# Optimization experiments

Hardware: AMD Instinct MI355X
Metric: run time of the kernel (lower is better)

The kernel has to match this reference:

```python
import jax, jax.numpy as jnp
import numpy as np

# Problem-size constants (match input_specs / init_kwargs)
B, D, H, W = 2, 128, 128, 128   # batch and spatial grid
N = 200_000                      # number of active (non-empty) voxels
CI, CO, K = 64, 64, 3            # channels and cubic kernel size
DIL = 1                          # dilation


def setup_inputs() -> dict:
    key = jax.random.key(0)
    k1, k2, k3 = jax.random.split(key, 3)
    # Unique active voxel coordinates (submanifold conv assumes unique sites).
    rng = np.random.default_rng(0)
    lin = rng.choice(B * D * H * W, size=N, replace=False)
    b, rem = np.divmod(lin, D * H * W)
    z, rem = np.divmod(rem, H * W)
    y, x = np.divmod(rem, W)
    coords = jnp.asarray(np.stack([b, z, y, x], axis=1).astype(np.int32))  # [N,4]
    feats = jax.random.normal(k1, (N, CI), dtype=jnp.float32)
    # kaiming-uniform-ish init, layout [Co, Kd, Kh, Kw, Ci] as in the module
    fan_in = CI * K * K * K
    bound = 1.0 / np.sqrt(fan_in)
    weight = jax.random.uniform(k2, (CO, K, K, K, CI), dtype=jnp.float32,
                                minval=-bound, maxval=bound)
    bias = jax.random.uniform(k3, (CO,), dtype=jnp.float32,
                              minval=-bound, maxval=bound)
    return {"feats": feats, "weight": weight, "bias": bias, "coords": coords}


def _build_grid(coords):
    """Dense voxel hash: linear cell id -> row index in feats (-1 if empty)."""
    n = coords.shape[0]
    lin = ((coords[:, 0] * D + coords[:, 1]) * H + coords[:, 2]) * W + coords[:, 3]
    grid = jnp.full((B * D * H * W,), -1, dtype=jnp.int32)
    return grid.at[lin].set(jnp.arange(n, dtype=jnp.int32))


def reference(feats, weight, bias, coords):
    # Submanifold sparse 3D conv: out[p] = bias + sum_k W[k] @ feats[p + dil*(k - center)]
    # (only where the neighbor voxel is active; output sites == input sites).
    n = feats.shape[0]
    grid = _build_grid(coords)
    c = K // 2
    bz, z0, y0, x0 = coords[:, 0], coords[:, 1], coords[:, 2], coords[:, 3]
    out = jnp.broadcast_to(bias.astype(feats.dtype), (n, CO))
    for kd in range(K):
        for kh in range(K):
            for kw in range(K):
                dz, dy, dx = DIL * (kd - c), DIL * (kh - c), DIL * (kw - c)
                nz, ny, nx = z0 + dz, y0 + dy, x0 + dx
                inb = (nz >= 0) & (nz < D) & (ny >= 0) & (ny < H) & (nx >= 0) & (nx < W)
                nlin = ((bz * D + jnp.clip(nz, 0, D - 1)) * H
                        + jnp.clip(ny, 0, H - 1)) * W + jnp.clip(nx, 0, W - 1)
                nidx = jnp.where(inb, grid[nlin], -1)          # rulebook for this offset
                valid = (nidx >= 0)[:, None]
                g = jnp.where(valid, feats[jnp.clip(nidx, 0)], 0.0)  # gather [N,Ci]
                out = out + jnp.einsum('nc,oc->no', g, weight[:, kd, kh, kw, :])
    return out
```

## Files before the change

### kernel.cpp

```cpp
#include <hip/hip_runtime.h>
#include <hip/hip_bf16.h>

#define BDIM 2
#define DDIM 128
#define HDIM 128
#define WDIM 128
#define CI 64
#define CO 64
#define NTAPS 27
#define GRID_CELLS (BDIM * DDIM * HDIM * WDIM)
#define NCBLK (GRID_CELLS / 256)

typedef __attribute__((ext_vector_type(8))) short short8;
typedef __attribute__((ext_vector_type(4))) float floatx4;

#define WT_OFF   ((size_t)16 << 20)
#define BCNT_OFF (WT_OFF + ((size_t)256 << 10))
#define ORD_OFF  (BCNT_OFF + ((size_t)64 << 10))

__device__ __forceinline__ unsigned short f2bf(float f) {
    unsigned int u = __float_as_uint(f);
    return (unsigned short)((u + 0x7FFFu + ((u >> 16) & 1u)) >> 16);
}

__global__ __launch_bounds__(256) void scatter_kernel(
    const int* __restrict__ coords, int* __restrict__ grid, int n) {
    int i = blockIdx.x * blockDim.x + threadIdx.x;
    if (i >= n) return;
    int4 c = ((const int4*)coords)[i];
    grid[((c.x * DDIM + c.y) * HDIM + c.z) * WDIM + c.w] = i;
}

__global__ __launch_bounds__(256) void wfrag_kernel(
    const float* __restrict__ weight, short8* __restrict__ wt8) {
    int idx = blockIdx.x * blockDim.x + threadIdx.x;
    if (idx >= NTAPS * 2 * 4 * 64) return;
    int l = idx & 63, ot = (idx >> 6) & 3, s = (idx >> 8) & 1, t = idx >> 9;
    int o = ot * 16 + (l & 15);
    int k0 = s * 32 + ((l >> 4) << 3);
    const float* src = weight + ((size_t)o * NTAPS + t) * CI + k0;
    short8 v;
#pragma unroll
    for (int j = 0; j < 8; ++j) v[j] = (short)f2bf(src[j]);
    wt8[idx] = v;
}

__global__ __launch_bounds__(256) void count_kernel(
    const int* __restrict__ grid, int* __restrict__ bcnt) {
    int i = blockIdx.x * 256 + threadIdx.x;
    unsigned long long b = __ballot(grid[i] >= 0);
    __shared__ int wc[4];
    if ((threadIdx.x & 63) == 0) wc[threadIdx.x >> 6] = __popcll(b);
    __syncthreads();
    if (threadIdx.x == 0) bcnt[blockIdx.x] = wc[0] + wc[1] + wc[2] + wc[3];
}

__global__ __launch_bounds__(1024) void scan_kernel(int* __restrict__ bcnt) {
    __shared__ int part[1024];
    int tid = threadIdx.x;
    int v[16], s = 0;
#pragma unroll
    for (int k = 0; k < 16; ++k) { v[k] = bcnt[tid * 16 + k]; s += v[k]; }
    part[tid] = s;
    __syncthreads();
    for (int off = 1; off < 1024; off <<= 1) {
        int t = (tid >= off) ? part[tid - off] : 0;
        __syncthreads();
        part[tid] += t;
        __syncthreads();
    }
    int ex = tid ? part[tid - 1] : 0;
#pragma unroll
    for (int k = 0; k < 16; ++k) { int nv = ex; ex += v[k]; bcnt[tid * 16 + k] = nv; }
}

__global__ __launch_bounds__(256) void emit_kernel(
    const int* __restrict__ grid, const int* __restrict__ boff,
    int* __restrict__ order) {
    int i = blockIdx.x * 256 + threadIdx.x;
    int v = grid[i];
    int lane = threadIdx.x & 63, w = threadIdx.x >> 6;
    unsigned long long b = __ballot(v >= 0);
    __shared__ int wc[4];
    if (lane == 0) wc[w] = __popcll(b);
    __syncthreads();
    int woff = 0;
    for (int k = 0; k < w; ++k) woff += wc[k];
    if (v >= 0) {
        int rank = __popcll(b & ((1ull << lane) - 1ull));
        order[boff[blockIdx.x] + woff + rank] = v;
    }
}

__global__ __launch_bounds__(256) void conv_kernel(
    const float* __restrict__ feats, const short8* __restrict__ wt8,
    const float* __restrict__ bias, const int* __restrict__ coords,
    const int* __restrict__ grid, const int* __restrict__ order,
    float* __restrict__ out, int n) {
    __shared__ short8 bs[3][512];
    int tid = threadIdx.x;
    int w = tid >> 6, l = tid & 63, quad = l >> 4, m = l & 15;
    int jrow = blockIdx.x * 64 + w * 16 + m;
    int j = jrow < n ? jrow : n - 1;
    int p = order[j];
    int4 c = ((const int4*)coords)[p];

    int pr[7];
#pragma unroll
    for (int i = 0; i < 7; ++i) {
        int t = 4 * i + quad;
        int v = -1;
        if (t < NTAPS) {
            int dz = t / 9 - 1, rem = t % 9;
            int dy = rem / 3 - 1, dx = rem % 3 - 1;
            int nz = c.y + dz, ny = c.z + dy, nx = c.w + dx;
            if (nz >= 0 && nz < DDIM && ny >= 0 && ny < HDIM &&
                nx >= 0 && nx < WDIM)
                v = grid[((c.x * DDIM + nz) * HDIM + ny) * WDIM + nx];
        }
        pr[i] = v;
    }

    floatx4 acc0 = {0.f, 0.f, 0.f, 0.f}, acc1 = acc0, acc2 = acc0, acc3 = acc0;
    float4 xA[4], xB[4];
    int vA = -1, vB = -1;

#define STAGE(t)                                                     \
    {                                                                \
        const short8* src = wt8 + (size_t)(t) * 512 + tid * 2;       \
        short8 s0 = src[0], s1 = src[1];                             \
        bs[(t) % 3][tid * 2] = s0;                                   \
        bs[(t) % 3][tid * 2 + 1] = s1;                               \
    }

#define GATHER(t, g, vv)                                             \
    {                                                                \
        int vsrc = pr[(t) >> 2];                                     \
        vv = __shfl(vsrc, (((t) & 3) << 4) | m);                     \
        g[0] = g[1] = g[2] = g[3] = float4{0.f, 0.f, 0.f, 0.f};      \
        if (vv >= 0) {                                               \
            const float4* ar =                                       \
                (const float4*)(feats + (size_t)vv * CI + quad * 8); \
            g[0] = ar[0]; g[1] = ar[1]; g[2] = ar[8]; g[3] = ar[9];  \
        }                                                            \
    }

#define COMPUTE(t, g, vv)                                                          \
    if (__ballot(vv >= 0) != 0ull) {                                               \
        union { short8 s; __hip_bfloat162 h[4]; } f0, f1;                          \
        f0.h[0] = __float22bfloat162_rn({g[0].x, g[0].y});                         \
        f0.h[1] = __float22bfloat162_rn({g[0].z, g[0].w});                         \
        f0.h[2] = __float22bfloat162_rn({g[1].x, g[1].y});                         \
        f0.h[3] = __float22bfloat162_rn({g[1].z, g[1].w});                         \
        f1.h[0] = __float22bfloat162_rn({g[2].x, g[2].y});                         \
        f1.h[1] = __float22bfloat162_rn({g[2].z, g[2].w});                         \
        f1.h[2] = __float22bfloat162_rn({g[3].x, g[3].y});                         \
        f1.h[3] = __float22bfloat162_rn({g[3].z, g[3].w});                         \
        const short8* wb = &bs[(t) % 3][l];                                        \
        acc0 = __builtin_amdgcn_mfma_f32_16x16x32_bf16(f0.s, wb[0 * 64], acc0, 0, 0, 0); \
        acc1 = __builtin_amdgcn_mfma_f32_16x16x32_bf16(f0.s, wb[1 * 64], acc1, 0, 0, 0); \
        acc2 = __builtin_amdgcn_mfma_f32_16x16x32_bf16(f0.s, wb[2 * 64], acc2, 0, 0, 0); \
        acc3 = __builtin_amdgcn_mfma_f32_16x16x32_bf16(f0.s, wb[3 * 64], acc3, 0, 0, 0); \
        acc0 = __builtin_amdgcn_mfma_f32_16x16x32_bf16(f1.s, wb[4 * 64], acc0, 0, 0, 0); \
        acc1 = __builtin_amdgcn_mfma_f32_16x16x32_bf16(f1.s, wb[5 * 64], acc1, 0, 0, 0); \
        acc2 = __builtin_amdgcn_mfma_f32_16x16x32_bf16(f1.s, wb[6 * 64], acc2, 0, 0, 0); \
        acc3 = __builtin_amdgcn_mfma_f32_16x16x32_bf16(f1.s, wb[7 * 64], acc3, 0, 0, 0); \
    }

    STAGE(0);
    GATHER(0, xA, vA);
#pragma unroll
    for (int t = 0; t < NTAPS; ++t) {
        if (t + 1 < NTAPS) {
            STAGE(t + 1);
            if (t & 1) { GATHER(t + 1, xA, vA); } else { GATHER(t + 1, xB, vB); }
        }
        __syncthreads();
        if (t & 1) { COMPUTE(t, xB, vB); } else { COMPUTE(t, xA, vA); }
    }

    float b0 = bias[m], b1 = bias[m + 16], b2 = bias[m + 32], b3 = bias[m + 48];
#pragma unroll
    for (int r = 0; r < 4; ++r) {
        int row = quad * 4 + r;
        int jr = blockIdx.x * 64 + w * 16 + row;
        int prow = __shfl(p, row);
        if (jr < n) {
            float* orow = out + (size_t)prow * CO;
            orow[m]      = acc0[r] + b0;
            orow[m + 16] = acc1[r] + b1;
            orow[m + 32] = acc2[r] + b2;
            orow[m + 48] = acc3[r] + b3;
        }
    }
#undef STAGE
#undef GATHER
#undef COMPUTE
}

extern "C" void kernel_launch(void* const* d_in, const int* in_sizes, int n_in,
                              void* d_out, int out_size, void* d_ws, size_t ws_size,
                              hipStream_t stream) {
    const float* feats  = (const float*)d_in[0];
    const float* weight = (const float*)d_in[1];
    const float* bias   = (const float*)d_in[2];
    const int*   coords = (const int*)d_in[3];
    float* out = (float*)d_out;
    int n = in_sizes[3] / 4;

    int*    grid  = (int*)d_ws;
    short8* wt8   = (short8*)((char*)d_ws + WT_OFF);
    int*    bcnt  = (int*)((char*)d_ws + BCNT_OFF);
    int*    order = (int*)((char*)d_ws + ORD_OFF);

    (void)hipMemsetAsync(grid, 0xFF, (size_t)GRID_CELLS * sizeof(int), stream);
    scatter_kernel<<<(n + 255) / 256, 256, 0, stream>>>(coords, grid, n);
    wfrag_kernel<<<(NTAPS * 2 * 4 * 64 + 255) / 256, 256, 0, stream>>>(weight, wt8);
    count_kernel<<<NCBLK, 256, 0, stream>>>(grid, bcnt);
    scan_kernel<<<1, 1024, 0, stream>>>(bcnt);
    emit_kernel<<<NCBLK, 256, 0, stream>>>(grid, bcnt, order);
    conv_kernel<<<(n + 63) / 64, 256, 0, stream>>>(
        feats, wt8, bias, coords, grid, order, out, n);
}
```

Measured before the change: 195.8 us.

## Pre-permute features to sorted bf16 buffer and remap grid to sorted ranks

The emit kernel now rewrites the voxel grid to hold sorted ranks, and a new kernel gathers features into a contiguous bf16 buffer in sorted order. The conv kernel then reads half-width, spatially coherent rows instead of scattered fp32 rows that each need conversion. The conv block grows to 512 threads with 7 taps of weights staged per group in place of a per-tap triple-buffered pipeline. This adds an extra pass over the features and more shared memory, and it loses the overlap of gathers with compute.

```diff
diff --git a/kernel.cpp b/kernel.cpp
--- a/kernel.cpp
+++ b/kernel.cpp
@@ -17,6 +17,7 @@
 #define WT_OFF   ((size_t)16 << 20)
 #define BCNT_OFF (WT_OFF + ((size_t)256 << 10))
 #define ORD_OFF  (BCNT_OFF + ((size_t)64 << 10))
+#define FS_OFF   (ORD_OFF + ((size_t)1 << 20))
 
 __device__ __forceinline__ unsigned short f2bf(float f) {
     unsigned int u = __float_as_uint(f);
@@ -75,7 +76,7 @@
 }
 
 __global__ __launch_bounds__(256) void emit_kernel(
-    const int* __restrict__ grid, const int* __restrict__ boff,
+    const int* __restrict__ boff, int* __restrict__ grid,
     int* __restrict__ order) {
     int i = blockIdx.x * 256 + threadIdx.x;
     int v = grid[i];
@@ -86,21 +87,36 @@
     __syncthreads();
     int woff = 0;
     for (int k = 0; k < w; ++k) woff += wc[k];
+    int rank = -1;
     if (v >= 0) {
-        int rank = __popcll(b & ((1ull << lane) - 1ull));
-        order[boff[blockIdx.x] + woff + rank] = v;
-    }
-}
-
-__global__ __launch_bounds__(256) void conv_kernel(
-    const float* __restrict__ feats, const short8* __restrict__ wt8,
-    const float* __restrict__ bias, const int* __restrict__ coords,
-    const int* __restrict__ grid, const int* __restrict__ order,
-    float* __restrict__ out, int n) {
-    __shared__ short8 bs[3][512];
+        rank = boff[blockIdx.x] + woff + __popcll(b & ((1ull << lane) - 1ull));
+        order[rank] = v;
+    }
+    grid[i] = rank;
+}
+
+__global__ __launch_bounds__(256) void fperm_kernel(
+    const float* __restrict__ feats, const int* __restrict__ order,
+    unsigned int* __restrict__ fso, int n) {
+    int row = blockIdx.x * 8 + (threadIdx.x >> 5);
+    if (row >= n) return;
+    int sub = threadIdx.x & 31;
+    int p = order[row];
+    float2 v = ((const float2*)(feats + (size_t)p * CI))[sub];
+    __hip_bfloat162 b = __float22bfloat162_rn(float2{v.x, v.y});
+    fso[(size_t)row * 32 + sub] = *(unsigned int*)&b;
+}
+
+template <bool USE_FS>
+__global__ __launch_bounds__(512, 4) void conv_kernel(
+    const float* __restrict__ feats, const short* __restrict__ fs,
+    const short8* __restrict__ wt8, const float* __restrict__ bias,
+    const int* __restrict__ coords, const int* __restrict__ rgrid,
+    const int* __restrict__ order, float* __restrict__ out, int n) {
+    __shared__ short8 bs[7 * 512];
     int tid = threadIdx.x;
     int w = tid >> 6, l = tid & 63, quad = l >> 4, m = l & 15;
-    int jrow = blockIdx.x * 64 + w * 16 + m;
+    int jrow = blockIdx.x * 128 + w * 16 + m;
     int j = jrow < n ? jrow : n - 1;
     int p = order[j];
     int4 c = ((const int4*)coords)[p];
@@ -116,74 +132,77 @@
             int nz = c.y + dz, ny = c.z + dy, nx = c.w + dx;
             if (nz >= 0 && nz < DDIM && ny >= 0 && ny < HDIM &&
                 nx >= 0 && nx < WDIM)
-                v = grid[((c.x * DDIM + nz) * HDIM + ny) * WDIM + nx];
+                v = rgrid[((c.x * DDIM + nz) * HDIM + ny) * WDIM + nx];
         }
         pr[i] = v;
     }
 
     floatx4 acc0 = {0.f, 0.f, 0.f, 0.f}, acc1 = acc0, acc2 = acc0, acc3 = acc0;
-    float4 xA[4], xB[4];
-    int vA = -1, vB = -1;
-
-#define STAGE(t)                                                     \
-    {                                                                \
-        const short8* src = wt8 + (size_t)(t) * 512 + tid * 2;       \
-        short8 s0 = src[0], s1 = src[1];                             \
-        bs[(t) % 3][tid * 2] = s0;                                   \
-        bs[(t) % 3][tid * 2 + 1] = s1;                               \
-    }
-
-#define GATHER(t, g, vv)                                             \
-    {                                                                \
-        int vsrc = pr[(t) >> 2];                                     \
-        vv = __shfl(vsrc, (((t) & 3) << 4) | m);                     \
-        g[0] = g[1] = g[2] = g[3] = float4{0.f, 0.f, 0.f, 0.f};      \
-        if (vv >= 0) {                                               \
-            const float4* ar =                                       \
-                (const float4*)(feats + (size_t)vv * CI + quad * 8); \
-            g[0] = ar[0]; g[1] = ar[1]; g[2] = ar[8]; g[3] = ar[9];  \
-        }                                                            \
-    }
-
-#define COMPUTE(t, g, vv)                                                          \
-    if (__ballot(vv >= 0) != 0ull) {                                               \
-        union { short8 s; __hip_bfloat162 h[4]; } f0, f1;                          \
-        f0.h[0] = __float22bfloat162_rn({g[0].x, g[0].y});                         \
-        f0.h[1] = __float22bfloat162_rn({g[0].z, g[0].w});                         \
-        f0.h[2] = __float22bfloat162_rn({g[1].x, g[1].y});                         \
-        f0.h[3] = __float22bfloat162_rn({g[1].z, g[1].w});                         \
-        f1.h[0] = __float22bfloat162_rn({g[2].x, g[2].y});                         \
-        f1.h[1] = __float22bfloat162_rn({g[2].z, g[2].w});                         \
-        f1.h[2] = __float22bfloat162_rn({g[3].x, g[3].y});                         \
-        f1.h[3] = __float22bfloat162_rn({g[3].z, g[3].w});                         \
-        const short8* wb = &bs[(t) % 3][l];                                        \
-        acc0 = __builtin_amdgcn_mfma_f32_16x16x32_bf16(f0.s, wb[0 * 64], acc0, 0, 0, 0); \
-        acc1 = __builtin_amdgcn_mfma_f32_16x16x32_bf16(f0.s, wb[1 * 64], acc1, 0, 0, 0); \
-        acc2 = __builtin_amdgcn_mfma_f32_16x16x32_bf16(f0.s, wb[2 * 64], acc2, 0, 0, 0); \
-        acc3 = __builtin_amdgcn_mfma_f32_16x16x32_bf16(f0.s, wb[3 * 64], acc3, 0, 0, 0); \
-        acc0 = __builtin_amdgcn_mfma_f32_16x16x32_bf16(f1.s, wb[4 * 64], acc0, 0, 0, 0); \
-        acc1 = __builtin_amdgcn_mfma_f32_16x16x32_bf16(f1.s, wb[5 * 64], acc1, 0, 0, 0); \
-        acc2 = __builtin_amdgcn_mfma_f32_16x16x32_bf16(f1.s, wb[6 * 64], acc2, 0, 0, 0); \
-        acc3 = __builtin_amdgcn_mfma_f32_16x16x32_bf16(f1.s, wb[7 * 64], acc3, 0, 0, 0); \
-    }
-
-    STAGE(0);
-    GATHER(0, xA, vA);
-#pragma unroll
-    for (int t = 0; t < NTAPS; ++t) {
-        if (t + 1 < NTAPS) {
-            STAGE(t + 1);
-            if (t & 1) { GATHER(t + 1, xA, vA); } else { GATHER(t + 1, xB, vB); }
-        }
-        __syncthreads();
-        if (t & 1) { COMPUTE(t, xB, vB); } else { COMPUTE(t, xA, vA); }
-    }
+
+#define STAGE_GRP(T0, SZ)                                            \
+    __syncthreads();                                                 \
+    for (int i = tid; i < (SZ) * 512; i += 512)                      \
+        bs[i] = wt8[(T0) * 512 + i];                                 \
+    __syncthreads();
+
+#define TAP(T, T0)                                                                 \
+    {                                                                              \
+        int rk = __shfl(pr[(T) >> 2], (((T) & 3) << 4) | m);                       \
+        if (__ballot(rk >= 0) != 0ull) {                                           \
+            short8 a0 = {0, 0, 0, 0, 0, 0, 0, 0};                                  \
+            short8 a1 = {0, 0, 0, 0, 0, 0, 0, 0};                                  \
+            if (rk >= 0) {                                                         \
+                if (USE_FS) {                                                      \
+                    const short8* ar = (const short8*)(fs + (size_t)rk * CI);      \
+                    a0 = ar[quad];                                                 \
+                    a1 = ar[quad + 4];                                             \
+                } else {                                                           \
+                    int op = order[rk];                                            \
+                    const float4* ar =                                             \
+                        (const float4*)(feats + (size_t)op * CI + quad * 8);       \
+                    float4 x0 = ar[0], x1 = ar[1], x2 = ar[8], x3 = ar[9];         \
+                    union { short8 sv; __hip_bfloat162 hv[4]; } u0, u1;            \
+                    u0.hv[0] = __float22bfloat162_rn(float2{x0.x, x0.y});          \
+                    u0.hv[1] = __float22bfloat162_rn(float2{x0.z, x0.w});          \
+                    u0.hv[2] = __float22bfloat162_rn(float2{x1.x, x1.y});          \
+                    u0.hv[3] = __float22bfloat162_rn(float2{x1.z, x1.w});          \
+                    u1.hv[0] = __float22bfloat162_rn(float2{x2.x, x2.y});          \
+                    u1.hv[1] = __float22bfloat162_rn(float2{x2.z, x2.w});          \
+                    u1.hv[2] = __float22bfloat162_rn(float2{x3.x, x3.y});          \
+                    u1.hv[3] = __float22bfloat162_rn(float2{x3.z, x3.w});          \
+                    a0 = u0.sv;                                                    \
+                    a1 = u1.sv;                                                    \
+                }                                                                  \
+            }                                                                      \
+            const short8* wb = bs + ((T) - (T0)) * 512 + l;                        \
+            acc0 = __builtin_amdgcn_mfma_f32_16x16x32_bf16(a0, wb[0 * 64], acc0, 0, 0, 0); \
+            acc1 = __builtin_amdgcn_mfma_f32_16x16x32_bf16(a0, wb[1 * 64], acc1, 0, 0, 0); \
+            acc2 = __builtin_amdgcn_mfma_f32_16x16x32_bf16(a0, wb[2 * 64], acc2, 0, 0, 0); \
+            acc3 = __builtin_amdgcn_mfma_f32_16x16x32_bf16(a0, wb[3 * 64], acc3, 0, 0, 0); \
+            acc0 = __builtin_amdgcn_mfma_f32_16x16x32_bf16(a1, wb[4 * 64], acc0, 0, 0, 0); \
+            acc1 = __builtin_amdgcn_mfma_f32_16x16x32_bf16(a1, wb[5 * 64], acc1, 0, 0, 0); \
+            acc2 = __builtin_amdgcn_mfma_f32_16x16x32_bf16(a1, wb[6 * 64], acc2, 0, 0, 0); \
+            acc3 = __builtin_amdgcn_mfma_f32_16x16x32_bf16(a1, wb[7 * 64], acc3, 0, 0, 0); \
+        }                                                                          \
+    }
+
+    STAGE_GRP(0, 7)
+    TAP(0, 0) TAP(1, 0) TAP(2, 0) TAP(3, 0) TAP(4, 0) TAP(5, 0) TAP(6, 0)
+    STAGE_GRP(7, 7)
+    TAP(7, 7) TAP(8, 7) TAP(9, 7) TAP(10, 7) TAP(11, 7) TAP(12, 7) TAP(13, 7)
+    STAGE_GRP(14, 7)
+    TAP(14, 14) TAP(15, 14) TAP(16, 14) TAP(17, 14) TAP(18, 14) TAP(19, 14) TAP(20, 14)
+    STAGE_GRP(21, 6)
+    TAP(21, 21) TAP(22, 21) TAP(23, 21) TAP(24, 21) TAP(25, 21) TAP(26, 21)
+
+#undef STAGE_GRP
+#undef TAP
 
     float b0 = bias[m], b1 = bias[m + 16], b2 = bias[m + 32], b3 = bias[m + 48];
 #pragma unroll
     for (int r = 0; r < 4; ++r) {
         int row = quad * 4 + r;
-        int jr = blockIdx.x * 64 + w * 16 + row;
+        int jr = blockIdx.x * 128 + w * 16 + row;
         int prow = __shfl(p, row);
         if (jr < n) {
             float* orow = out + (size_t)prow * CO;
@@ -193,9 +212,6 @@
             orow[m + 48] = acc3[r] + b3;
         }
     }
-#undef STAGE
-#undef GATHER
-#undef COMPUTE
 }
 
 extern "C" void kernel_launch(void* const* d_in, const int* in_sizes, int n_in,
@@ -212,13 +228,23 @@
     short8* wt8   = (short8*)((char*)d_ws + WT_OFF);
     int*    bcnt  = (int*)((char*)d_ws + BCNT_OFF);
     int*    order = (int*)((char*)d_ws + ORD_OFF);
+    short*  fs    = (short*)((char*)d_ws + FS_OFF);
+
+    bool use_fs = ws_size >= FS_OFF + (size_t)n * CI * sizeof(short);
 
     (void)hipMemsetAsync(grid, 0xFF, (size_t)GRID_CELLS * sizeof(int), stream);
     scatter_kernel<<<(n + 255) / 256, 256, 0, stream>>>(coords, grid, n);
     wfrag_kernel<<<(NTAPS * 2 * 4 * 64 + 255) / 256, 256, 0, stream>>>(weight, wt8);
     count_kernel<<<NCBLK, 256, 0, stream>>>(grid, bcnt);
     scan_kernel<<<1, 1024, 0, stream>>>(bcnt);
-    emit_kernel<<<NCBLK, 256, 0, stream>>>(grid, bcnt, order);
-    conv_kernel<<<(n + 63) / 64, 256, 0, stream>>>(
-        feats, wt8, bias, coords, grid, order, out, n);
-}
+    emit_kernel<<<NCBLK, 256, 0, stream>>>(bcnt, grid, order);
+    int cblocks = (n + 127) / 128;
+    if (use_fs) {
+        fperm_kernel<<<(n + 7) / 8, 256, 0, stream>>>(feats, order, (unsigned int*)fs, n);
+        conv_kernel<true><<<cblocks, 512, 0, stream>>>(
+            feats, fs, wt8, bias, coords, grid, order, out, n);
+    } else {
+        conv_kernel<false><<<cblocks, 512, 0, stream>>>(
+            feats, fs, wt8, bias, coords, grid, order, out, n);
+    }
+}
```

After: 221.6 us. 13.1% more time.
